# Kernel tuning notes

Measured on AMD Instinct MI355X. Metric: run time of the kernel, lower is better.

The kernel has to match this reference:

```python
import jax, jax.numpy as jnp
import numpy as np

B, CIN, T = 32, 64, 4096
E, H, HD, FF, L = 256, 8, 32, 1024, 4
K, S = 15, 2
SEQ = 512
GROUPS = E // 2
EPS = 1e-5


def setup_inputs() -> dict:
    key = jax.random.key(0)
    ks = jax.random.split(key, 16)
    d = {}
    d['x'] = jax.random.normal(ks[0], (B, CIN, T), jnp.float32)
    d['conv0_w'] = jax.random.normal(ks[1], (E, CIN, K), jnp.float32) * 0.03
    d['conv0_b'] = jnp.zeros((E,), jnp.float32)
    d['conv12_w'] = jax.random.normal(ks[2], (2, E, E, K), jnp.float32) * 0.016
    d['conv12_b'] = jnp.zeros((2, E), jnp.float32)
    d['gn_g'] = jnp.ones((3, E), jnp.float32)
    d['gn_b'] = jnp.zeros((3, E), jnp.float32)
    d['Wq'] = jax.random.normal(ks[3], (L, H, HD, E), jnp.float32) * 0.0625
    d['Wk'] = jax.random.normal(ks[4], (L, H, HD, E), jnp.float32) * 0.0625
    d['Wv'] = jax.random.normal(ks[5], (L, H, HD, E), jnp.float32) * 0.0625
    d['Wo'] = jax.random.normal(ks[6], (L, E, E), jnp.float32) * 0.0625
    d['ln1_g'] = jnp.ones((L, E), jnp.float32)
    d['ln1_b'] = jnp.zeros((L, E), jnp.float32)
    d['Wf1'] = jax.random.normal(ks[7], (L, FF, E), jnp.float32) * 0.0625
    d['bf1'] = jnp.zeros((L, FF), jnp.float32)
    d['Wf2'] = jax.random.normal(ks[8], (L, E, FF), jnp.float32) * 0.03125
    d['bf2'] = jnp.zeros((L, E), jnp.float32)
    d['ln2_g'] = jnp.ones((L, E), jnp.float32)
    d['ln2_b'] = jnp.zeros((L, E), jnp.float32)
    d['Wc1'] = jax.random.normal(ks[9], (256, SEQ * E), jnp.float32) * 0.003
    d['bc1'] = jnp.zeros((256,), jnp.float32)
    d['Wc2'] = jax.random.normal(ks[10], (1, 256), jnp.float32) * 0.0625
    d['bc2'] = jnp.zeros((1,), jnp.float32)
    return d


def conv1d(x, w, b, stride, pad):
    y = jax.lax.conv_general_dilated(x, w, (stride,), [(pad, pad)],
                                     dimension_numbers=('NCH', 'OIH', 'NCH'))
    return y + b[None, :, None]


def group_norm(x, g, b):
    # x: [B, C, Len]; torch GroupNorm with C//2 groups
    Bn, C, Ln = x.shape
    xg = x.reshape(Bn, GROUPS, C // GROUPS, Ln)
    mu = xg.mean(axis=(2, 3), keepdims=True)
    var = ((xg - mu) ** 2).mean(axis=(2, 3), keepdims=True)
    xn = ((xg - mu) * jax.lax.rsqrt(var + EPS)).reshape(Bn, C, Ln)
    return xn * g[None, :, None] + b[None, :, None]


def layer_norm(x, g, b):
    mu = x.mean(-1, keepdims=True)
    var = ((x - mu) ** 2).mean(-1, keepdims=True)
    return (x - mu) * jax.lax.rsqrt(var + EPS) * g + b


def pos_encoding(seq, e):
    t = jnp.arange(seq, dtype=jnp.float32)[:, None]
    i = jnp.arange(e, dtype=jnp.float32)[None, :]
    ang = t / jnp.power(10000.0, i / e)  # note: i/e, matching the source
    return jnp.where(jnp.arange(e)[None, :] % 2 == 0, jnp.sin(ang), jnp.cos(ang))


def reference(x, conv0_w, conv0_b, conv12_w, conv12_b, gn_g, gn_b,
              Wq, Wk, Wv, Wo, ln1_g, ln1_b, Wf1, bf1, Wf2, bf2,
              ln2_g, ln2_b, Wc1, bc1, Wc2, bc2):
    # --- conv encoder: (conv -> dropout(eval) -> groupnorm -> gelu) x3 ---
    h = conv1d(x, conv0_w, conv0_b, S, K // 2)
    h = jax.nn.gelu(group_norm(h, gn_g[0], gn_b[0]), approximate=False)
    for i in range(2):
        h = conv1d(h, conv12_w[i], conv12_b[i], S, K // 2)
        h = jax.nn.gelu(group_norm(h, gn_g[i + 1], gn_b[i + 1]), approximate=False)
    h = jnp.transpose(h, (0, 2, 1))  # [B, SEQ, E]

    # --- transformer encoder ---
    h = h + pos_encoding(h.shape[1], E)[None]
    scale = 1.0 / jnp.sqrt(jnp.float32(HD))
    for l in range(L):
        q = jnp.einsum('bse,hde->bhsd', h, Wq[l])
        k = jnp.einsum('bse,hde->bhsd', h, Wk[l])
        v = jnp.einsum('bse,hde->bhsd', h, Wv[l])
        attn = jax.nn.softmax(jnp.einsum('bhqd,bhkd->bhqk', q, k) * scale, axis=-1)
        o = jnp.einsum('bhqk,bhkd->bhqd', attn, v)
        o = jnp.transpose(o, (0, 2, 1, 3)).reshape(h.shape[0], h.shape[1], E)
        o = o @ Wo[l].T
        h1 = layer_norm(o + h, ln1_g[l], ln1_b[l])
        f = jax.nn.relu(h1 @ Wf1[l].T + bf1[l]) @ Wf2[l].T + bf2[l]
        h = layer_norm(f + h1, ln2_g[l], ln2_b[l])

    # --- binary classifier ---
    flat = h.reshape(h.shape[0], -1)  # [B, SEQ*E]
    hid = jax.nn.relu(flat @ Wc1.T + bc1)
    return jax.nn.sigmoid(hid @ Wc2.T + bc2)  # [B, 1]
```

## Files before the change

kernel.cpp:

```cpp
#include <hip/hip_runtime.h>
#include <math.h>


typedef unsigned int   u32;
typedef unsigned short u16;
typedef __attribute__((ext_vector_type(4))) float f32x4;
typedef __attribute__((ext_vector_type(8))) short bf16x8;

__device__ __forceinline__ u16 f2bf(float v) {
    union { float f; u32 u; } x; x.f = v;
    u32 r = x.u + 0x7fffu + ((x.u >> 16) & 1u);
    return (u16)(r >> 16);
}

__device__ __forceinline__ void gl2lds16(const void* gsrc, void* ldst) {
    __builtin_amdgcn_global_load_lds(
        (const __attribute__((address_space(1))) void*)gsrc,
        (__attribute__((address_space(3))) void*)ldst, 16, 0, 0);
}

__device__ __forceinline__ float maeeg_block_sum(float v, float* sc4) {
#pragma unroll
    for (int off = 32; off; off >>= 1) v += __shfl_down(v, off);
    int t = threadIdx.x;
    if ((t & 63) == 0) sc4[t >> 6] = v;
    __syncthreads();
    float r = sc4[0] + sc4[1] + sc4[2] + sc4[3];
    __syncthreads();
    return r;
}

__global__ __launch_bounds__(256) void maeeg_mm_kernel(
    const u16* __restrict__ Ag, const u16* __restrict__ Bg,
    const float* __restrict__ bias, const float* __restrict__ res,
    void* __restrict__ outp, int N, int K, int flags)
{
    __shared__ u16 As[8192];
    __shared__ u16 Bs[8192];
    const int m0 = blockIdx.x * 128, n0 = blockIdx.y * 128;
    const int t = threadIdx.x, w = t >> 6, lane = t & 63;
    const int fr = lane & 15, fq = lane >> 4;
    const int wm = (w >> 1) * 64, wn = (w & 1) * 64;
    const int srow = lane >> 3;
    const int srcc = (lane & 7) ^ srow;

    f32x4 acc[4][4];
    const f32x4 zero = {0.f, 0.f, 0.f, 0.f};
#pragma unroll
    for (int i = 0; i < 4; ++i)
#pragma unroll
        for (int j = 0; j < 4; ++j) acc[i][j] = zero;

    for (int k0 = 0; k0 < K; k0 += 64) {
#pragma unroll
        for (int j = 0; j < 4; ++j) {
            int rowb = w * 32 + j * 8;
            int r = rowb + srow;
            gl2lds16(Ag + (size_t)(m0 + r) * K + k0 + srcc * 8,
                     (char*)As + rowb * 128);
            gl2lds16(Bg + (size_t)(n0 + r) * K + k0 + srcc * 8,
                     (char*)Bs + rowb * 128);
        }
        __syncthreads();
#pragma unroll
        for (int kc = 0; kc < 2; ++kc) {
            bf16x8 af[4], bfv[4];
#pragma unroll
            for (int i = 0; i < 4; ++i) {
                int am = wm + i * 16 + fr;
                int bn = wn + i * 16 + fr;
                int kb = kc * 64 + fq * 16;
                af[i]  = *(const bf16x8*)((const char*)As + am * 128 + (kb ^ ((am & 7) << 4)));
                bfv[i] = *(const bf16x8*)((const char*)Bs + bn * 128 + (kb ^ ((bn & 7) << 4)));
            }
#pragma unroll
            for (int i = 0; i < 4; ++i)
#pragma unroll
                for (int j = 0; j < 4; ++j)
                    acc[i][j] = __builtin_amdgcn_mfma_f32_16x16x32_bf16(
                        af[i], bfv[j], acc[i][j], 0, 0, 0);
        }
        __syncthreads();
    }
#pragma unroll
    for (int i = 0; i < 4; ++i) {
#pragma unroll
        for (int j = 0; j < 4; ++j) {
            int n = n0 + wn + j * 16 + fr;
            float bv = bias ? bias[n] : 0.f;
#pragma unroll
            for (int r = 0; r < 4; ++r) {
                int m = m0 + wm + i * 16 + fq * 4 + r;
                float v = acc[i][j][r] + bv;
                if (res) v += res[(size_t)m * N + n];
                if (flags & 1) v = fmaxf(v, 0.f);
                if (flags & 16) {
                    u16* o = (u16*)outp;
                    int seg = n >> 8, nn = n & 255;
                    if (seg == 0)
                        o[(size_t)m * 256 + nn] = f2bf(v * 0.17677669529663687f);
                    else if (seg == 1)
                        o[4194304 + (size_t)m * 256 + nn] = f2bf(v);
                    else
                        o[8388608 + (((size_t)(m >> 9)) * 256 + nn) * 512 + (m & 511)] = f2bf(v);
                } else if (flags & 4)
                    ((u16*)outp)[(((size_t)(m >> 9)) * 256 + n) * 512 + (m & 511)] = f2bf(v);
                else if (flags & 2)
                    ((u16*)outp)[(size_t)m * N + n] = f2bf(v);
                else
                    ((float*)outp)[(size_t)m * N + n] = v;
            }
        }
    }
}

__global__ __launch_bounds__(256) void maeeg_convmm_kernel(
    const u16* __restrict__ Wp, const u16* __restrict__ inp,
    const float* __restrict__ cb, float* __restrict__ out,
    int K3, int len_in, int len_out)
{
    __shared__ u16 As[8192];
    __shared__ u16 Bs[8192];
    const int m0 = blockIdx.x * 128, t0 = blockIdx.y * 128, b = blockIdx.z;
    const int lip = len_in + 16;
    const u16* inb = inp + (size_t)b * (K3 >> 4) * lip;
    const int t = threadIdx.x, w = t >> 6, lane = t & 63;
    const int sr = lane & 7, sc = lane >> 3;
    const int fr = lane & 15, fq = lane >> 4;
    const int wm = (w >> 1) * 64, wn = (w & 1) * 64;
    const int srow = lane >> 3;
    const int srcc = (lane & 7) ^ srow;

    f32x4 acc[4][4];
    const f32x4 zero = {0.f, 0.f, 0.f, 0.f};
#pragma unroll
    for (int i = 0; i < 4; ++i)
#pragma unroll
        for (int j = 0; j < 4; ++j) acc[i][j] = zero;

    for (int k0 = 0; k0 < K3; k0 += 64) {
#pragma unroll
        for (int j = 0; j < 4; ++j) {
            int rowb = w * 32 + j * 8;
            gl2lds16(Wp + (size_t)(m0 + rowb + srow) * K3 + k0 + srcc * 8,
                     (char*)As + rowb * 128);
            int row = rowb + sr;
            int k  = k0 + sc * 8;
            int ci = k >> 4, rr = k & 15;
            int tg = t0 + row;
            const u16* gp = inb + (size_t)ci * lip + 2 * tg + rr;
            uint4 vb;
            vb.x = *(const u32*)(gp);
            vb.y = *(const u32*)(gp + 2);
            vb.z = *(const u32*)(gp + 4);
            vb.w = *(const u32*)(gp + 6);
            int kb = (sc ^ (row & 7)) << 4;
            *(uint4*)((char*)Bs + row * 128 + kb) = vb;
        }
        __syncthreads();
#pragma unroll
        for (int kc = 0; kc < 2; ++kc) {
            bf16x8 af[4], bfv[4];
#pragma unroll
            for (int i = 0; i < 4; ++i) {
                int am = wm + i * 16 + fr;
                int bn = wn + i * 16 + fr;
                int kb = kc * 64 + fq * 16;
                af[i]  = *(const bf16x8*)((const char*)As + am * 128 + (kb ^ ((am & 7) << 4)));
                bfv[i] = *(const bf16x8*)((const char*)Bs + bn * 128 + (kb ^ ((bn & 7) << 4)));
            }
#pragma unroll
            for (int i = 0; i < 4; ++i)
#pragma unroll
                for (int j = 0; j < 4; ++j)
                    acc[i][j] = __builtin_amdgcn_mfma_f32_16x16x32_bf16(
                        af[i], bfv[j], acc[i][j], 0, 0, 0);
        }
        __syncthreads();
    }
#pragma unroll
    for (int i = 0; i < 4; ++i) {
#pragma unroll
        for (int r = 0; r < 4; ++r) {
            int m = m0 + wm + i * 16 + fq * 4 + r;
            float bb = cb[m];
            float* op = out + ((size_t)b * 256 + m) * len_out + t0;
#pragma unroll
            for (int j = 0; j < 4; ++j)
                op[wn + j * 16 + fr] = acc[i][j][r] + bb;
        }
    }
}

__global__ __launch_bounds__(256) void maeeg_fattn_kernel(
    const u16* __restrict__ Qb, const u16* __restrict__ Kb,
    const u16* __restrict__ Vt, u16* __restrict__ att)
{
    __shared__ u16 Ks[64 * 32];
    __shared__ u16 Vs[32 * 64];
    __shared__ u16 Ps[4][32 * 64];
    const int qt = blockIdx.x, h = blockIdx.y, b = blockIdx.z;
    const int t = threadIdx.x, w = t >> 6, lane = t & 63;
    const int fr = lane & 15, fq = lane >> 4;
    const u16* qbase = Qb + (size_t)b * 512 * 256 + h * 32;
    const u16* kbase = Kb + (size_t)b * 512 * 256 + h * 32;
    const u16* vbase = Vt + (size_t)b * 256 * 512 + (size_t)h * 32 * 512;

    bf16x8 qf[2];
#pragma unroll
    for (int mi = 0; mi < 2; ++mi)
        qf[mi] = *(const bf16x8*)(qbase +
                 (size_t)(qt * 128 + w * 32 + mi * 16 + fr) * 256 + fq * 8);

    f32x4 oacc[2][2];
    const f32x4 zero = {0.f, 0.f, 0.f, 0.f};
    oacc[0][0] = zero; oacc[0][1] = zero; oacc[1][0] = zero; oacc[1][1] = zero;
    float mrun[8], lrun[8];
#pragma unroll
    for (int i = 0; i < 8; ++i) { mrun[i] = -1e30f; lrun[i] = 0.f; }

    for (int kt = 0; kt < 512; kt += 64) {
        {
            int row = t >> 2, c = t & 3;
            uint4 kv = *(const uint4*)(kbase + (size_t)(kt + row) * 256 + c * 8);
            *(uint4*)((char*)Ks + row * 64 + (((c ^ (row & 3)) << 4))) = kv;
            int d = t >> 3, c2 = t & 7;
            uint4 vv = *(const uint4*)(vbase + (size_t)d * 512 + kt + c2 * 8);
            *(uint4*)((char*)Vs + d * 128 + ((c2 ^ (d & 7)) << 4)) = vv;
        }
        __syncthreads();

        f32x4 sacc[2][4];
#pragma unroll
        for (int mi = 0; mi < 2; ++mi)
#pragma unroll
            for (int ni = 0; ni < 4; ++ni) sacc[mi][ni] = zero;
        bf16x8 kf[4];
#pragma unroll
        for (int ni = 0; ni < 4; ++ni) {
            int kk = ni * 16 + fr;
            kf[ni] = *(const bf16x8*)((const char*)Ks + kk * 64 +
                                      ((fq ^ (kk & 3)) << 4));
        }
#pragma unroll
        for (int mi = 0; mi < 2; ++mi)
#pragma unroll
            for (int ni = 0; ni < 4; ++ni)
                sacc[mi][ni] = __builtin_amdgcn_mfma_f32_16x16x32_bf16(
                    qf[mi], kf[ni], sacc[mi][ni], 0, 0, 0);

#pragma unroll
        for (int mi = 0; mi < 2; ++mi) {
#pragma unroll
            for (int reg = 0; reg < 4; ++reg) {
                int idx = mi * 4 + reg;
                float rm = fmaxf(fmaxf(sacc[mi][0][reg], sacc[mi][1][reg]),
                                 fmaxf(sacc[mi][2][reg], sacc[mi][3][reg]));
                rm = fmaxf(rm, __shfl_xor(rm, 1));
                rm = fmaxf(rm, __shfl_xor(rm, 2));
                rm = fmaxf(rm, __shfl_xor(rm, 4));
                rm = fmaxf(rm, __shfl_xor(rm, 8));
                float mold = mrun[idx];
                float mnew = fmaxf(mold, rm);
                float c = __expf(mold - mnew);
                mrun[idx] = mnew;
                int q = mi * 16 + fq * 4 + reg;
                float psum = 0.f;
#pragma unroll
                for (int ni = 0; ni < 4; ++ni) {
                    float p = __expf(sacc[mi][ni][reg] - mnew);
                    psum += p;
                    int kk = ni * 16 + fr;
                    int boff = q * 128 + ((((kk >> 3) ^ (q & 7)) << 4) | ((kk & 7) << 1));
                    *(u16*)((char*)Ps[w] + boff) = f2bf(p);
                }
                lrun[idx] = lrun[idx] * c + psum;
                oacc[mi][0][reg] *= c;
                oacc[mi][1][reg] *= c;
            }
        }

        bf16x8 pf[2][2], vf[2][2];
#pragma unroll
        for (int mi = 0; mi < 2; ++mi)
#pragma unroll
            for (int kc = 0; kc < 2; ++kc) {
                int q = mi * 16 + fr;
                int ch = (kc * 4 + fq) ^ (q & 7);
                pf[mi][kc] = *(const bf16x8*)((const char*)Ps[w] + q * 128 + (ch << 4));
            }
#pragma unroll
        for (int nj = 0; nj < 2; ++nj)
#pragma unroll
            for (int kc = 0; kc < 2; ++kc) {
                int d = nj * 16 + fr;
                int ch = (kc * 4 + fq) ^ (d & 7);
                vf[nj][kc] = *(const bf16x8*)((const char*)Vs + d * 128 + (ch << 4));
            }
#pragma unroll
        for (int mi = 0; mi < 2; ++mi)
#pragma unroll
            for (int nj = 0; nj < 2; ++nj) {
                oacc[mi][nj] = __builtin_amdgcn_mfma_f32_16x16x32_bf16(
                    pf[mi][0], vf[nj][0], oacc[mi][nj], 0, 0, 0);
                oacc[mi][nj] = __builtin_amdgcn_mfma_f32_16x16x32_bf16(
                    pf[mi][1], vf[nj][1], oacc[mi][nj], 0, 0, 0);
            }
        __syncthreads();
    }

#pragma unroll
    for (int idx = 0; idx < 8; ++idx) {
        float l = lrun[idx];
        l += __shfl_xor(l, 1);
        l += __shfl_xor(l, 2);
        l += __shfl_xor(l, 4);
        l += __shfl_xor(l, 8);
        lrun[idx] = 1.f / l;
    }
    u16* ob = att + (size_t)b * 512 * 256 + h * 32;
#pragma unroll
    for (int mi = 0; mi < 2; ++mi)
#pragma unroll
        for (int reg = 0; reg < 4; ++reg) {
            int q = qt * 128 + w * 32 + mi * 16 + fq * 4 + reg;
            float inv = lrun[mi * 4 + reg];
#pragma unroll
            for (int nj = 0; nj < 2; ++nj)
                ob[(size_t)q * 256 + nj * 16 + fr] =
                    f2bf(oacc[mi][nj][reg] * inv);
        }
}

__global__ void maeeg_prep_convw_kernel(const float* __restrict__ src,
                                        u16* __restrict__ dst, int nrows)
{
    int i = blockIdx.x * 256 + threadIdx.x;
    if (i >= nrows) return;
    const float* s = src + (size_t)i * 15;
    float4 a = *(const float4*)s;
    float4 b = *(const float4*)(s + 4);
    float4 c = *(const float4*)(s + 8);
    float e12 = s[12], e13 = s[13], e14 = s[14];
    uint4 p0, p1;
    p0.x = (u32)f2bf(a.x) | ((u32)f2bf(a.y) << 16);
    p0.y = (u32)f2bf(a.z) | ((u32)f2bf(a.w) << 16);
    p0.z = (u32)f2bf(b.x) | ((u32)f2bf(b.y) << 16);
    p0.w = (u32)f2bf(b.z) | ((u32)f2bf(b.w) << 16);
    p1.x = (u32)f2bf(c.x) | ((u32)f2bf(c.y) << 16);
    p1.y = (u32)f2bf(c.z) | ((u32)f2bf(c.w) << 16);
    p1.z = (u32)f2bf(e12) | ((u32)f2bf(e13) << 16);
    p1.w = (u32)f2bf(e14);
    uint4* d = (uint4*)(dst + (size_t)i * 16);
    d[0] = p0; d[1] = p1;
}

__global__ void maeeg_cast8_kernel(const float* __restrict__ src,
                                   u16* __restrict__ dst, int n8)
{
    int i = blockIdx.x * 256 + threadIdx.x;
    if (i >= n8) return;
    float4 a = ((const float4*)(src + (size_t)i * 8))[0];
    float4 b = ((const float4*)(src + (size_t)i * 8))[1];
    uint4 p;
    p.x = (u32)f2bf(a.x) | ((u32)f2bf(a.y) << 16);
    p.y = (u32)f2bf(a.z) | ((u32)f2bf(a.w) << 16);
    p.z = (u32)f2bf(b.x) | ((u32)f2bf(b.y) << 16);
    p.w = (u32)f2bf(b.z) | ((u32)f2bf(b.w) << 16);
    *(uint4*)(dst + (size_t)i * 8) = p;
}

__global__ void maeeg_cast_qkv_kernel(const float* __restrict__ src,
                                      u16* __restrict__ dst, int seg)
{
    int i = blockIdx.x * 256 + threadIdx.x;
    int l = i >> 13, r = (i & 8191) * 8;
    float4 a = ((const float4*)(src + (size_t)i * 8))[0];
    float4 b = ((const float4*)(src + (size_t)i * 8))[1];
    uint4 p;
    p.x = (u32)f2bf(a.x) | ((u32)f2bf(a.y) << 16);
    p.y = (u32)f2bf(a.z) | ((u32)f2bf(a.w) << 16);
    p.z = (u32)f2bf(b.x) | ((u32)f2bf(b.y) << 16);
    p.w = (u32)f2bf(b.z) | ((u32)f2bf(b.w) << 16);
    *(uint4*)(dst + (size_t)l * 196608 + seg * 65536 + r) = p;
}

__global__ void maeeg_cast_pad_kernel(const float* __restrict__ src,
                                      u16* __restrict__ dst, int len)
{
    int lip = len + 16;
    int n8 = lip >> 3;
    int i = blockIdx.x * 256 + threadIdx.x;
    if (i >= n8) return;
    int row = blockIdx.y;
    int p0 = i * 8;
    u16 vals[8];
#pragma unroll
    for (int e = 0; e < 8; ++e) {
        int q = p0 + e - 7;
        vals[e] = (q >= 0 && q < len) ? f2bf(src[(size_t)row * len + q]) : (u16)0;
    }
    uint4 pk;
    pk.x = (u32)vals[0] | ((u32)vals[1] << 16);
    pk.y = (u32)vals[2] | ((u32)vals[3] << 16);
    pk.z = (u32)vals[4] | ((u32)vals[5] << 16);
    pk.w = (u32)vals[6] | ((u32)vals[7] << 16);
    *(uint4*)(dst + (size_t)row * lip + p0) = pk;
}

__global__ void maeeg_pe_kernel(float* __restrict__ pet)
{
    int s = blockIdx.x, e = threadIdx.x;
    float ang = (float)s / powf(10000.f, (float)e * (1.f / 256.f));
    pet[s * 256 + e] = (e & 1) ? cosf(ang) : sinf(ang);
}

__global__ __launch_bounds__(256) void maeeg_gn_gelu_kernel(
    float* __restrict__ h, const float* __restrict__ g,
    const float* __restrict__ bta, int len, u16* __restrict__ bfout, int lip)
{
    const int grp = blockIdx.x, b = blockIdx.y;
    float* p = h + ((size_t)b * 256 + grp * 2) * len;
    const int n = 2 * len;
    float s1 = 0.f, s2 = 0.f;
    for (int i = threadIdx.x; i < n; i += 256) {
        float v = p[i];
        s1 += v; s2 += v * v;
    }
    __shared__ float sc[4];
    float S1 = maeeg_block_sum(s1, sc);
    float S2 = maeeg_block_sum(s2, sc);
    float mu = S1 / (float)n;
    float var = fmaxf(S2 / (float)n - mu * mu, 0.f);
    float rs = rsqrtf(var + 1e-5f);
    float g0 = g[grp * 2], g1 = g[grp * 2 + 1];
    float b0 = bta[grp * 2], b1 = bta[grp * 2 + 1];
    u16* bp = bfout ? bfout + ((size_t)b * 256 + grp * 2) * lip : (u16*)0;
    for (int i = threadIdx.x; i < n; i += 256) {
        float v = (p[i] - mu) * rs;
        float y = (i < len) ? (v * g0 + b0) : (v * g1 + b1);
        float ge = 0.5f * y * (1.f + erff(y * 0.70710678118654752f));
        p[i] = ge;
        if (bp) bp[(i < len ? i : (i - len) + lip) + 7] = f2bf(ge);
    }
    if (bp && threadIdx.x < 32) {
        int ch = threadIdx.x >> 4, pp = threadIdx.x & 15;
        bp[(size_t)ch * lip + ((pp < 7) ? pp : (len + pp))] = 0;
    }
}

__global__ __launch_bounds__(256) void maeeg_transpose_pos_kernel(
    const float* __restrict__ in, const float* __restrict__ pet,
    float* __restrict__ out, u16* __restrict__ outb)
{
    __shared__ float tile[256][33];
    const int s0 = blockIdx.x * 32, b = blockIdx.y;
    for (int idx = threadIdx.x; idx < 256 * 32; idx += 256) {
        int e = idx >> 5, j = idx & 31;
        tile[e][j] = in[((size_t)b * 256 + e) * 512 + s0 + j];
    }
    __syncthreads();
    for (int idx = threadIdx.x; idx < 32 * 256; idx += 256) {
        int j = idx >> 8, e = idx & 255;
        float v = tile[e][j] + pet[(s0 + j) * 256 + e];
        size_t o = ((size_t)b * 512 + s0 + j) * 256 + e;
        out[o] = v;
        outb[o] = f2bf(v);
    }
}

__global__ __launch_bounds__(256) void maeeg_ln_kernel(
    const float* __restrict__ in, float* __restrict__ out,
    u16* __restrict__ bfout, const float* __restrict__ g,
    const float* __restrict__ b)
{
    const int w = threadIdx.x >> 6, lane = threadIdx.x & 63;
    const size_t m = (size_t)blockIdx.x * 4 + w;
    const float4 v = *(const float4*)(in + m * 256 + lane * 4);
    float s = v.x + v.y + v.z + v.w;
#pragma unroll
    for (int off = 32; off; off >>= 1) s += __shfl_xor(s, off);
    float mu = s * (1.f / 256.f);
    float dx = v.x - mu, dy = v.y - mu, dz = v.z - mu, dw = v.w - mu;
    float q = dx * dx + dy * dy + dz * dz + dw * dw;
#pragma unroll
    for (int off = 32; off; off >>= 1) q += __shfl_xor(q, off);
    float rs = rsqrtf(q * (1.f / 256.f) + 1e-5f);
    float4 gg = *(const float4*)(g + lane * 4);
    float4 bb = *(const float4*)(b + lane * 4);
    float o0 = dx * rs * gg.x + bb.x;
    float o1 = dy * rs * gg.y + bb.y;
    float o2 = dz * rs * gg.z + bb.z;
    float o3 = dw * rs * gg.w + bb.w;
    *(float4*)(out + m * 256 + lane * 4) = make_float4(o0, o1, o2, o3);
    uint2 pk;
    pk.x = (u32)f2bf(o0) | ((u32)f2bf(o1) << 16);
    pk.y = (u32)f2bf(o2) | ((u32)f2bf(o3) << 16);
    *(uint2*)(bfout + m * 256 + lane * 4) = pk;
}

__global__ __launch_bounds__(256) void maeeg_cls1_kernel(
    const u16* __restrict__ flatb, const float* __restrict__ Wc1,
    float* __restrict__ part)
{
    __shared__ u16 As[32 * 64];
    __shared__ u16 Bs[64 * 64];
    const int ks = blockIdx.x, jt = blockIdx.y;
    const int t = threadIdx.x, w = t >> 6, lane = t & 63;
    const int fr = lane & 15, fq = lane >> 4;
    const int kbase0 = ks * 1024;
    const int brow = t >> 2, bq = t & 3;
    const int srow = lane >> 3;
    const int srcc = (lane & 7) ^ srow;

    f32x4 acc[2];
    const f32x4 zero = {0.f, 0.f, 0.f, 0.f};
    acc[0] = zero; acc[1] = zero;

    for (int step = 0; step < 16; ++step) {
        int kk = kbase0 + step * 64;
        int rowb = w * 8;
        gl2lds16(flatb + (size_t)(rowb + srow) * 131072 + kk + srcc * 8,
                 (char*)As + rowb * 128);
        const float* wp = Wc1 + (size_t)(jt * 64 + brow) * 131072 + kk + bq * 16;
        float4 f0 = ((const float4*)wp)[0];
        float4 f1 = ((const float4*)wp)[1];
        float4 f2 = ((const float4*)wp)[2];
        float4 f3 = ((const float4*)wp)[3];
        uint4 p0, p1;
        p0.x = (u32)f2bf(f0.x) | ((u32)f2bf(f0.y) << 16);
        p0.y = (u32)f2bf(f0.z) | ((u32)f2bf(f0.w) << 16);
        p0.z = (u32)f2bf(f1.x) | ((u32)f2bf(f1.y) << 16);
        p0.w = (u32)f2bf(f1.z) | ((u32)f2bf(f1.w) << 16);
        p1.x = (u32)f2bf(f2.x) | ((u32)f2bf(f2.y) << 16);
        p1.y = (u32)f2bf(f2.z) | ((u32)f2bf(f2.w) << 16);
        p1.z = (u32)f2bf(f3.x) | ((u32)f2bf(f3.y) << 16);
        p1.w = (u32)f2bf(f3.z) | ((u32)f2bf(f3.w) << 16);
        int c0 = bq * 2, c1 = bq * 2 + 1;
        *(uint4*)((char*)Bs + brow * 128 + ((c0 ^ (brow & 7)) << 4)) = p0;
        *(uint4*)((char*)Bs + brow * 128 + ((c1 ^ (brow & 7)) << 4)) = p1;
        __syncthreads();
#pragma unroll
        for (int kc = 0; kc < 2; ++kc) {
            int kbyte = kc * 64 + fq * 16;
            int bn = w * 16 + fr;
            bf16x8 bfv = *(const bf16x8*)((const char*)Bs + bn * 128 +
                                          (kbyte ^ ((bn & 7) << 4)));
#pragma unroll
            for (int mi = 0; mi < 2; ++mi) {
                int am = mi * 16 + fr;
                bf16x8 af = *(const bf16x8*)((const char*)As + am * 128 +
                                             (kbyte ^ ((am & 7) << 4)));
                acc[mi] = __builtin_amdgcn_mfma_f32_16x16x32_bf16(
                    af, bfv, acc[mi], 0, 0, 0);
            }
        }
        __syncthreads();
    }
#pragma unroll
    for (int mi = 0; mi < 2; ++mi)
#pragma unroll
        for (int r = 0; r < 4; ++r) {
            int m = mi * 16 + fq * 4 + r;
            int j = jt * 64 + w * 16 + fr;
            part[((size_t)ks * 32 + m) * 256 + j] = acc[mi][r];
        }
}

__global__ __launch_bounds__(256) void maeeg_cls23_kernel(
    const float* __restrict__ part, const float* __restrict__ bc1,
    const float* __restrict__ Wc2, const float* __restrict__ bc2,
    float* __restrict__ out)
{
    const int b = blockIdx.x, j = threadIdx.x;
    float s = bc1[j];
    for (int ks = 0; ks < 128; ++ks) s += part[((size_t)ks * 32 + b) * 256 + j];
    float v = fmaxf(s, 0.f) * Wc2[j];
    __shared__ float sc[4];
    float tot = maeeg_block_sum(v, sc);
    if (j == 0) out[b] = 1.f / (1.f + expf(-(tot + bc2[0])));
}

extern "C" void kernel_launch(void* const* d_in, const int* in_sizes, int n_in,
                              void* d_out, int out_size, void* d_ws, size_t ws_size,
                              hipStream_t stream)
{
    (void)in_sizes; (void)n_in; (void)out_size; (void)ws_size;
    const float* x        = (const float*)d_in[0];
    const float* conv0_w  = (const float*)d_in[1];
    const float* conv0_b  = (const float*)d_in[2];
    const float* conv12_w = (const float*)d_in[3];
    const float* conv12_b = (const float*)d_in[4];
    const float* gn_g     = (const float*)d_in[5];
    const float* gn_b     = (const float*)d_in[6];
    const float* Wq       = (const float*)d_in[7];
    const float* Wk       = (const float*)d_in[8];
    const float* Wv       = (const float*)d_in[9];
    const float* Wo       = (const float*)d_in[10];
    const float* ln1_g    = (const float*)d_in[11];
    const float* ln1_b    = (const float*)d_in[12];
    const float* Wf1      = (const float*)d_in[13];
    const float* bf1      = (const float*)d_in[14];
    const float* Wf2      = (const float*)d_in[15];
    const float* bf2      = (const float*)d_in[16];
    const float* ln2_g    = (const float*)d_in[17];
    const float* ln2_b    = (const float*)d_in[18];
    const float* Wc1      = (const float*)d_in[19];
    const float* bc1      = (const float*)d_in[20];
    const float* Wc2      = (const float*)d_in[21];
    const float* bc2      = (const float*)d_in[22];
    float* out = (float*)d_out;

    char* wsb = (char*)d_ws;
    u16* WB0   = (u16*)(wsb + 0);
    u16* WB12  = (u16*)(wsb + 524288);
    u16* WQKVb = (u16*)(wsb + 4718592);
    u16* WOb   = (u16*)(wsb + 6291456);
    u16* WF1b  = (u16*)(wsb + 6815744);
    u16* WF2b  = (u16*)(wsb + 8912896);
    u16*   XPAD  = (u16*)(wsb + 11010048);
    u16*   GN1B  = (u16*)(wsb + 11010048);
    float* D     = (float*)(wsb + 11010048);
    float* CONV0 = (float*)(wsb + 28049408);
    float* CONV1 = (float*)(wsb + 28049408);
    float* CONV2 = (float*)(wsb + 28049408 + 33554432);
    u16*   Qb2   = (u16*)(wsb + 28049408);
    u16*   ATTb  = (u16*)(wsb + 28049408 + 25165824);
    u16*   Db    = (u16*)(wsb + 28049408 + 33554432);
    u16*   F1b   = (u16*)(wsb + 28049408);
    u16*   GN0B  = (u16*)(wsb + 95158272);
    float* C     = (float*)(wsb + 95158272);
    u16*   Cb    = (u16*)(wsb + 95158272 + 16777216);
    float* PART  = (float*)(wsb + 128974848);
    float* HID   = (float*)(wsb + 133169152);
    float* PET   = (float*)(wsb + 133201920);
    (void)HID;

    maeeg_prep_convw_kernel<<<64, 256, 0, stream>>>(conv0_w, WB0, 16384);
    maeeg_prep_convw_kernel<<<512, 256, 0, stream>>>(conv12_w, WB12, 131072);
    maeeg_cast_qkv_kernel<<<128, 256, 0, stream>>>(Wq, WQKVb, 0);
    maeeg_cast_qkv_kernel<<<128, 256, 0, stream>>>(Wk, WQKVb, 1);
    maeeg_cast_qkv_kernel<<<128, 256, 0, stream>>>(Wv, WQKVb, 2);
    maeeg_cast8_kernel<<<128, 256, 0, stream>>>(Wo, WOb, 32768);
    maeeg_cast8_kernel<<<512, 256, 0, stream>>>(Wf1, WF1b, 131072);
    maeeg_cast8_kernel<<<512, 256, 0, stream>>>(Wf2, WF2b, 131072);
    maeeg_cast_pad_kernel<<<dim3(3, 2048), 256, 0, stream>>>(x, XPAD, 4096);
    maeeg_pe_kernel<<<512, 256, 0, stream>>>(PET);

    maeeg_convmm_kernel<<<dim3(2, 16, 32), 256, 0, stream>>>(
        WB0, XPAD, conv0_b, CONV0, 1024, 4096, 2048);
    maeeg_gn_gelu_kernel<<<dim3(128, 32), 256, 0, stream>>>(
        CONV0, gn_g, gn_b, 2048, GN0B, 2064);
    maeeg_convmm_kernel<<<dim3(2, 8, 32), 256, 0, stream>>>(
        WB12, GN0B, conv12_b, CONV1, 4096, 2048, 1024);
    maeeg_gn_gelu_kernel<<<dim3(128, 32), 256, 0, stream>>>(
        CONV1, gn_g + 256, gn_b + 256, 1024, GN1B, 1040);
    maeeg_convmm_kernel<<<dim3(2, 4, 32), 256, 0, stream>>>(
        WB12 + 256 * 4096, GN1B, conv12_b + 256, CONV2, 4096, 1024, 512);
    maeeg_gn_gelu_kernel<<<dim3(128, 32), 256, 0, stream>>>(
        CONV2, gn_g + 512, gn_b + 512, 512, (u16*)0, 0);
    maeeg_transpose_pos_kernel<<<dim3(16, 32), 256, 0, stream>>>(CONV2, PET, C, Cb);

    for (int l = 0; l < 4; ++l) {
        maeeg_mm_kernel<<<dim3(128, 6), 256, 0, stream>>>(
            Cb, WQKVb + l * 196608, (const float*)0, (const float*)0,
            Qb2, 256, 256, 16);
        maeeg_fattn_kernel<<<dim3(4, 8, 32), 256, 0, stream>>>(
            Qb2, Qb2 + 4194304, Qb2 + 8388608, ATTb);
        maeeg_mm_kernel<<<dim3(128, 2), 256, 0, stream>>>(
            ATTb, WOb + l * 65536, (const float*)0, C, D, 256, 256, 0);
        maeeg_ln_kernel<<<4096, 256, 0, stream>>>(
            D, D, Db, ln1_g + l * 256, ln1_b + l * 256);
        maeeg_mm_kernel<<<dim3(128, 8), 256, 0, stream>>>(
            Db, WF1b + l * 262144, bf1 + l * 1024, (const float*)0, F1b, 1024, 256, 3);
        maeeg_mm_kernel<<<dim3(128, 2), 256, 0, stream>>>(
            F1b, WF2b + l * 262144, bf2 + l * 256, D, C, 256, 1024, 0);
        maeeg_ln_kernel<<<4096, 256, 0, stream>>>(
            C, C, Cb, ln2_g + l * 256, ln2_b + l * 256);
    }

    maeeg_cls1_kernel<<<dim3(128, 4), 256, 0, stream>>>(Cb, Wc1, PART);
    maeeg_cls23_kernel<<<32, 256, 0, stream>>>(PART, bc1, Wc2, bc2, out);
}
```

Baseline: 1.122 ms.

## Fuse Wo/FF2 GEMMs with residual add and LayerNorm; merge weight cast launches

Adds a GEMM kernel in which each block computes 64 full rows of 256 columns, so residual add, bias and LayerNorm can be applied in the epilogue using shared-memory partial row sums. This replaces the separate mm and ln kernels after the attention output projection and after FF2, removing fp32 round trips and launches. Weight bf16 casts are merged into two launches. Unneeded fp32 writes are skipped for the first two GroupNorm layers and the last layer output. The fused kernel's 64-row tiles give fewer, larger blocks, which may lower GEMM parallelism.

```diff
diff --git a/kernel.cpp b/kernel.cpp
--- a/kernel.cpp
+++ b/kernel.cpp
@@ -114,6 +114,117 @@
     }
 }
 
+__global__ __launch_bounds__(512) void maeeg_mmln_kernel(
+    const u16* __restrict__ Ag, const u16* __restrict__ Bg,
+    const float* __restrict__ bias, const float* __restrict__ res,
+    const float* __restrict__ g, const float* __restrict__ b,
+    float* __restrict__ outf, u16* __restrict__ outb, int K)
+{
+    __shared__ u16 As[64 * 64];
+    __shared__ u16 Bs[256 * 64];
+    __shared__ float psum[64][4];
+    __shared__ float psq[64][4];
+    const int m0 = blockIdx.x * 64;
+    const int t = threadIdx.x, w = t >> 6, lane = t & 63;
+    const int fr = lane & 15, fq = lane >> 4;
+    const int wm = (w & 1) * 32, wn = (w >> 1) * 64;
+    const int seg = w >> 1;
+    const int srow = lane >> 3;
+    const int srcc = (lane & 7) ^ srow;
+
+    f32x4 acc[2][4];
+    const f32x4 zero = {0.f, 0.f, 0.f, 0.f};
+#pragma unroll
+    for (int i = 0; i < 2; ++i)
+#pragma unroll
+        for (int j = 0; j < 4; ++j) acc[i][j] = zero;
+
+    for (int k0 = 0; k0 < K; k0 += 64) {
+        gl2lds16(Ag + (size_t)(m0 + w * 8 + srow) * K + k0 + srcc * 8,
+                 (char*)As + (w * 8) * 128);
+#pragma unroll
+        for (int j = 0; j < 4; ++j) {
+            int rowb = w * 32 + j * 8;
+            gl2lds16(Bg + (size_t)(rowb + srow) * K + k0 + srcc * 8,
+                     (char*)Bs + rowb * 128);
+        }
+        __syncthreads();
+#pragma unroll
+        for (int kc = 0; kc < 2; ++kc) {
+            int kb = kc * 64 + fq * 16;
+            bf16x8 af[2], bfv[4];
+#pragma unroll
+            for (int i = 0; i < 2; ++i) {
+                int am = wm + i * 16 + fr;
+                af[i] = *(const bf16x8*)((const char*)As + am * 128 + (kb ^ ((am & 7) << 4)));
+            }
+#pragma unroll
+            for (int j = 0; j < 4; ++j) {
+                int bn = wn + j * 16 + fr;
+                bfv[j] = *(const bf16x8*)((const char*)Bs + bn * 128 + (kb ^ ((bn & 7) << 4)));
+            }
+#pragma unroll
+            for (int i = 0; i < 2; ++i)
+#pragma unroll
+                for (int j = 0; j < 4; ++j)
+                    acc[i][j] = __builtin_amdgcn_mfma_f32_16x16x32_bf16(
+                        af[i], bfv[j], acc[i][j], 0, 0, 0);
+        }
+        __syncthreads();
+    }
+
+#pragma unroll
+    for (int j = 0; j < 4; ++j) {
+        int n = wn + j * 16 + fr;
+        float bv = bias ? bias[n] : 0.f;
+#pragma unroll
+        for (int i = 0; i < 2; ++i)
+#pragma unroll
+            for (int r = 0; r < 4; ++r) {
+                int m = m0 + wm + i * 16 + fq * 4 + r;
+                acc[i][j][r] += bv + res[(size_t)m * 256 + n];
+            }
+    }
+#pragma unroll
+    for (int i = 0; i < 2; ++i)
+#pragma unroll
+        for (int r = 0; r < 4; ++r) {
+            float s = acc[i][0][r] + acc[i][1][r] + acc[i][2][r] + acc[i][3][r];
+            float q = acc[i][0][r] * acc[i][0][r] + acc[i][1][r] * acc[i][1][r]
+                    + acc[i][2][r] * acc[i][2][r] + acc[i][3][r] * acc[i][3][r];
+#pragma unroll
+            for (int off = 1; off < 16; off <<= 1) {
+                s += __shfl_xor(s, off);
+                q += __shfl_xor(q, off);
+            }
+            if (fr == 0) {
+                int ml = wm + i * 16 + fq * 4 + r;
+                psum[ml][seg] = s;
+                psq[ml][seg] = q;
+            }
+        }
+    __syncthreads();
+#pragma unroll
+    for (int i = 0; i < 2; ++i)
+#pragma unroll
+        for (int r = 0; r < 4; ++r) {
+            int ml = wm + i * 16 + fq * 4 + r;
+            float S = psum[ml][0] + psum[ml][1] + psum[ml][2] + psum[ml][3];
+            float Q = psq[ml][0] + psq[ml][1] + psq[ml][2] + psq[ml][3];
+            float mu = S * (1.f / 256.f);
+            float var = fmaxf(Q * (1.f / 256.f) - mu * mu, 0.f);
+            float rs = rsqrtf(var + 1e-5f);
+            size_t mrow = (size_t)(m0 + ml) * 256;
+#pragma unroll
+            for (int j = 0; j < 4; ++j) {
+                int n = wn + j * 16 + fr;
+                float o = (acc[i][j][r] - mu) * rs * g[n] + b[n];
+                if (outf) outf[mrow + n] = o;
+                outb[mrow + n] = f2bf(o);
+            }
+        }
+}
+
 __global__ __launch_bounds__(256) void maeeg_convmm_kernel(
     const u16* __restrict__ Wp, const u16* __restrict__ inp,
     const float* __restrict__ cb, float* __restrict__ out,
@@ -355,34 +466,40 @@
     d[0] = p0; d[1] = p1;
 }
 
-__global__ void maeeg_cast8_kernel(const float* __restrict__ src,
-                                   u16* __restrict__ dst, int n8)
-{
-    int i = blockIdx.x * 256 + threadIdx.x;
-    if (i >= n8) return;
-    float4 a = ((const float4*)(src + (size_t)i * 8))[0];
-    float4 b = ((const float4*)(src + (size_t)i * 8))[1];
+__device__ __forceinline__ uint4 pack8(const float* s) {
+    float4 a = ((const float4*)s)[0];
+    float4 b = ((const float4*)s)[1];
     uint4 p;
     p.x = (u32)f2bf(a.x) | ((u32)f2bf(a.y) << 16);
     p.y = (u32)f2bf(a.z) | ((u32)f2bf(a.w) << 16);
     p.z = (u32)f2bf(b.x) | ((u32)f2bf(b.y) << 16);
     p.w = (u32)f2bf(b.z) | ((u32)f2bf(b.w) << 16);
-    *(uint4*)(dst + (size_t)i * 8) = p;
-}
-
-__global__ void maeeg_cast_qkv_kernel(const float* __restrict__ src,
-                                      u16* __restrict__ dst, int seg)
-{
+    return p;
+}
+
+__global__ void maeeg_cast_www_kernel(
+    const float* __restrict__ Wo, u16* __restrict__ dWo,
+    const float* __restrict__ Wf1, u16* __restrict__ dWf1,
+    const float* __restrict__ Wf2, u16* __restrict__ dWf2)
+{
+    int i = blockIdx.x * 256 + threadIdx.x;
+    const float* s; u16* d; int off;
+    if (i < 32768)       { s = Wo;  d = dWo;  off = i; }
+    else if (i < 163840) { s = Wf1; d = dWf1; off = i - 32768; }
+    else                 { s = Wf2; d = dWf2; off = i - 163840; }
+    *(uint4*)(d + (size_t)off * 8) = pack8(s + (size_t)off * 8);
+}
+
+__global__ void maeeg_cast_qkv3_kernel(
+    const float* __restrict__ Wq, const float* __restrict__ Wk,
+    const float* __restrict__ Wv, u16* __restrict__ dst)
+{
+    int seg = blockIdx.y;
+    const float* src = (seg == 0) ? Wq : ((seg == 1) ? Wk : Wv);
     int i = blockIdx.x * 256 + threadIdx.x;
     int l = i >> 13, r = (i & 8191) * 8;
-    float4 a = ((const float4*)(src + (size_t)i * 8))[0];
-    float4 b = ((const float4*)(src + (size_t)i * 8))[1];
-    uint4 p;
-    p.x = (u32)f2bf(a.x) | ((u32)f2bf(a.y) << 16);
-    p.y = (u32)f2bf(a.z) | ((u32)f2bf(a.w) << 16);
-    p.z = (u32)f2bf(b.x) | ((u32)f2bf(b.y) << 16);
-    p.w = (u32)f2bf(b.z) | ((u32)f2bf(b.w) << 16);
-    *(uint4*)(dst + (size_t)l * 196608 + seg * 65536 + r) = p;
+    *(uint4*)(dst + (size_t)l * 196608 + seg * 65536 + r) =
+        pack8(src + (size_t)i * 8);
 }
 
 __global__ void maeeg_cast_pad_kernel(const float* __restrict__ src,
@@ -417,7 +534,8 @@
 
 __global__ __launch_bounds__(256) void maeeg_gn_gelu_kernel(
     float* __restrict__ h, const float* __restrict__ g,
-    const float* __restrict__ bta, int len, u16* __restrict__ bfout, int lip)
+    const float* __restrict__ bta, int len, u16* __restrict__ bfout, int lip,
+    int keep32)
 {
     const int grp = blockIdx.x, b = blockIdx.y;
     float* p = h + ((size_t)b * 256 + grp * 2) * len;
@@ -440,7 +558,7 @@
         float v = (p[i] - mu) * rs;
         float y = (i < len) ? (v * g0 + b0) : (v * g1 + b1);
         float ge = 0.5f * y * (1.f + erff(y * 0.70710678118654752f));
-        p[i] = ge;
+        if (keep32) p[i] = ge;
         if (bp) bp[(i < len ? i : (i - len) + lip) + 7] = f2bf(ge);
     }
     if (bp && threadIdx.x < 32) {
@@ -467,36 +585,6 @@
         out[o] = v;
         outb[o] = f2bf(v);
     }
-}
-
-__global__ __launch_bounds__(256) void maeeg_ln_kernel(
-    const float* __restrict__ in, float* __restrict__ out,
-    u16* __restrict__ bfout, const float* __restrict__ g,
-    const float* __restrict__ b)
-{
-    const int w = threadIdx.x >> 6, lane = threadIdx.x & 63;
-    const size_t m = (size_t)blockIdx.x * 4 + w;
-    const float4 v = *(const float4*)(in + m * 256 + lane * 4);
-    float s = v.x + v.y + v.z + v.w;
-#pragma unroll
-    for (int off = 32; off; off >>= 1) s += __shfl_xor(s, off);
-    float mu = s * (1.f / 256.f);
-    float dx = v.x - mu, dy = v.y - mu, dz = v.z - mu, dw = v.w - mu;
-    float q = dx * dx + dy * dy + dz * dz + dw * dw;
-#pragma unroll
-    for (int off = 32; off; off >>= 1) q += __shfl_xor(q, off);
-    float rs = rsqrtf(q * (1.f / 256.f) + 1e-5f);
-    float4 gg = *(const float4*)(g + lane * 4);
-    float4 bb = *(const float4*)(b + lane * 4);
-    float o0 = dx * rs * gg.x + bb.x;
-    float o1 = dy * rs * gg.y + bb.y;
-    float o2 = dz * rs * gg.z + bb.z;
-    float o3 = dw * rs * gg.w + bb.w;
-    *(float4*)(out + m * 256 + lane * 4) = make_float4(o0, o1, o2, o3);
-    uint2 pk;
-    pk.x = (u32)f2bf(o0) | ((u32)f2bf(o1) << 16);
-    pk.y = (u32)f2bf(o2) | ((u32)f2bf(o3) << 16);
-    *(uint2*)(bfout + m * 256 + lane * 4) = pk;
 }
 
 __global__ __launch_bounds__(256) void maeeg_cls1_kernel(
@@ -632,33 +720,27 @@
     float* C     = (float*)(wsb + 95158272);
     u16*   Cb    = (u16*)(wsb + 95158272 + 16777216);
     float* PART  = (float*)(wsb + 128974848);
-    float* HID   = (float*)(wsb + 133169152);
     float* PET   = (float*)(wsb + 133201920);
-    (void)HID;
 
     maeeg_prep_convw_kernel<<<64, 256, 0, stream>>>(conv0_w, WB0, 16384);
     maeeg_prep_convw_kernel<<<512, 256, 0, stream>>>(conv12_w, WB12, 131072);
-    maeeg_cast_qkv_kernel<<<128, 256, 0, stream>>>(Wq, WQKVb, 0);
-    maeeg_cast_qkv_kernel<<<128, 256, 0, stream>>>(Wk, WQKVb, 1);
-    maeeg_cast_qkv_kernel<<<128, 256, 0, stream>>>(Wv, WQKVb, 2);
-    maeeg_cast8_kernel<<<128, 256, 0, stream>>>(Wo, WOb, 32768);
-    maeeg_cast8_kernel<<<512, 256, 0, stream>>>(Wf1, WF1b, 131072);
-    maeeg_cast8_kernel<<<512, 256, 0, stream>>>(Wf2, WF2b, 131072);
+    maeeg_cast_qkv3_kernel<<<dim3(128, 3), 256, 0, stream>>>(Wq, Wk, Wv, WQKVb);
+    maeeg_cast_www_kernel<<<1152, 256, 0, stream>>>(Wo, WOb, Wf1, WF1b, Wf2, WF2b);
     maeeg_cast_pad_kernel<<<dim3(3, 2048), 256, 0, stream>>>(x, XPAD, 4096);
     maeeg_pe_kernel<<<512, 256, 0, stream>>>(PET);
 
     maeeg_convmm_kernel<<<dim3(2, 16, 32), 256, 0, stream>>>(
         WB0, XPAD, conv0_b, CONV0, 1024, 4096, 2048);
     maeeg_gn_gelu_kernel<<<dim3(128, 32), 256, 0, stream>>>(
-        CONV0, gn_g, gn_b, 2048, GN0B, 2064);
+        CONV0, gn_g, gn_b, 2048, GN0B, 2064, 0);
     maeeg_convmm_kernel<<<dim3(2, 8, 32), 256, 0, stream>>>(
         WB12, GN0B, conv12_b, CONV1, 4096, 2048, 1024);
     maeeg_gn_gelu_kernel<<<dim3(128, 32), 256, 0, stream>>>(
-        CONV1, gn_g + 256, gn_b + 256, 1024, GN1B, 1040);
+        CONV1, gn_g + 256, gn_b + 256, 1024, GN1B, 1040, 0);
     maeeg_convmm_kernel<<<dim3(2, 4, 32), 256, 0, stream>>>(
         WB12 + 256 * 4096, GN1B, conv12_b + 256, CONV2, 4096, 1024, 512);
     maeeg_gn_gelu_kernel<<<dim3(128, 32), 256, 0, stream>>>(
-        CONV2, gn_g + 512, gn_b + 512, 512, (u16*)0, 0);
+        CONV2, gn_g + 512, gn_b + 512, 512, (u16*)0, 0, 1);
     maeeg_transpose_pos_kernel<<<dim3(16, 32), 256, 0, stream>>>(CONV2, PET, C, Cb);
 
     for (int l = 0; l < 4; ++l) {
@@ -667,16 +749,14 @@
             Qb2, 256, 256, 16);
         maeeg_fattn_kernel<<<dim3(4, 8, 32), 256, 0, stream>>>(
             Qb2, Qb2 + 4194304, Qb2 + 8388608, ATTb);
-        maeeg_mm_kernel<<<dim3(128, 2), 256, 0, stream>>>(
-            ATTb, WOb + l * 65536, (const float*)0, C, D, 256, 256, 0);
-        maeeg_ln_kernel<<<4096, 256, 0, stream>>>(
-            D, D, Db, ln1_g + l * 256, ln1_b + l * 256);
+        maeeg_mmln_kernel<<<256, 512, 0, stream>>>(
+            ATTb, WOb + l * 65536, (const float*)0, C,
+            ln1_g + l * 256, ln1_b + l * 256, D, Db, 256);
         maeeg_mm_kernel<<<dim3(128, 8), 256, 0, stream>>>(
             Db, WF1b + l * 262144, bf1 + l * 1024, (const float*)0, F1b, 1024, 256, 3);
-        maeeg_mm_kernel<<<dim3(128, 2), 256, 0, stream>>>(
-            F1b, WF2b + l * 262144, bf2 + l * 256, D, C, 256, 1024, 0);
-        maeeg_ln_kernel<<<4096, 256, 0, stream>>>(
-            C, C, Cb, ln2_g + l * 256, ln2_b + l * 256);
+        maeeg_mmln_kernel<<<256, 512, 0, stream>>>(
+            F1b, WF2b + l * 262144, bf2 + l * 256, D,
+            ln2_g + l * 256, ln2_b + l * 256, (l == 3) ? (float*)0 : C, Cb, 1024);
     }
 
     maeeg_cls1_kernel<<<dim3(128, 4), 256, 0, stream>>>(Cb, Wc1, PART);
```

Result: faster. 941.4 us (-16.1%).
